# Kernel optimization log

Measured on AMD Instinct MI355X. Metric: run time of the kernel, lower is better.

## Reference

```python
import jax, jax.numpy as jnp
import numpy as np


def _segsum(x):
    """Stable segment sum: exp(segsum(A)) is 1-semiseparable. x: (..., T) -> (..., T, T)."""
    T = x.shape[-1]
    xx = jnp.broadcast_to(x[..., None], (*x.shape, T))
    xx = jnp.where(jnp.tril(jnp.ones((T, T), bool), -1), xx, 0.0)
    s = jnp.cumsum(xx, axis=-2)
    return jnp.where(jnp.tril(jnp.ones((T, T), bool), 0), s, -jnp.inf)


def setup_inputs() -> dict:
    key = jax.random.key(0)
    ks = jax.random.split(key, 6)
    b, T, h, p, n = 2, 1024, 32, 64, 128
    x = jax.random.normal(ks[0], (b, T, h, p), jnp.float32)
    # negative decay rates, as produced by -exp(A_log)*softplus(dt) in Mamba2
    A = -jax.random.uniform(ks[1], (b, T, h), jnp.float32, minval=0.01, maxval=0.5)
    B = jax.random.normal(ks[2], (b, T, h, n), jnp.float32)
    C = jax.random.normal(ks[3], (b, T, h, n), jnp.float32)
    # retrieval similarity mask (lower-triangular, like segment_and_cosine_similarity output)
    L_mask = jax.random.uniform(ks[4], (b, h, T, T), jnp.float32) * jnp.tril(jnp.ones((T, T), jnp.float32))
    mask_scaling_factor = jnp.float32(0.5)
    return {"x": x, "A": A, "B": B, "C": C, "L_mask": L_mask,
            "mask_scaling_factor": mask_scaling_factor, "chunk_size": 64}


def reference(x, A, B, C, L_mask, mask_scaling_factor, chunk_size):
    b, T, h, p = x.shape
    n = B.shape[-1]
    l = chunk_size
    k = T // l
    # chunk: b (c l) ... -> b c l ...
    xr = x.reshape(b, k, l, h, p)
    Br = B.reshape(b, k, l, h, n)
    Cr = C.reshape(b, k, l, h, n)
    Ar = jnp.transpose(A.reshape(b, k, l, h), (0, 3, 1, 2))  # b h c l
    A_cs = jnp.cumsum(Ar, axis=-1)                            # b h c l
    L = jnp.exp(_segsum(Ar))                                  # b h c l l
    # decompose_diagonal_and_lower_tri(L_mask, chunk_size)
    r = L_mask.reshape(b, h, k, l, k, l)
    didx = np.arange(k)
    L_mask_diag = jnp.moveaxis(r[:, :, didx, :, didx, :], 0, 2)          # b h k l l
    row_idx, col_idx = np.tril_indices(k, -1)                             # strict lower block pairs
    lower_tri = jnp.moveaxis(r[:, :, row_idx, :, col_idx, :], 0, 2)       # b h P l l
    L = L + mask_scaling_factor * L_mask_diag
    # diagonal (intra-chunk) blocks
    Y_diag = jnp.einsum('bclhn,bcshn,bhcls,bcshp->bclhp', Cr, Br, L, xr)
    # retrieval off-diagonal blocks, scatter-added back per destination chunk
    Y_tmp = jnp.einsum('bclhn,bcshn,bhcls,bcshp->bclhp',
                       Cr[:, row_idx], Br[:, col_idx],
                       mask_scaling_factor * lower_tri, xr[:, col_idx])   # b P l h p
    Y_retr = jnp.moveaxis(
        jax.ops.segment_sum(jnp.moveaxis(Y_tmp, 1, 0), jnp.asarray(row_idx), num_segments=k),
        0, 1)                                                             # b k l h p
    # inter-chunk state passing
    decay_states = jnp.exp(A_cs[..., -1:] - A_cs)                         # b h c l
    states = jnp.einsum('bclhn,bhcl,bclhp->bchpn', Br, decay_states, xr)  # b c h p n
    states = jnp.concatenate([jnp.zeros_like(states[:, :1]), states], axis=1)
    decay_chunk = jnp.exp(_segsum(jnp.pad(A_cs[..., -1], ((0, 0), (0, 0), (1, 0)))))  # b h (k+1) (k+1)
    new_states = jnp.einsum('bhzc,bchpn->bzhpn', decay_chunk, states)
    states_in, final_state = new_states[:, :-1], new_states[:, -1]
    Y_off = jnp.einsum('bclhn,bchpn,bhcl->bclhp', Cr, states_in, jnp.exp(A_cs))
    Y = (Y_diag + Y_off + Y_retr).reshape(b, T, h, p)
    return Y, final_state
```

## Files before the change

kernel.cpp:

```cpp
#include <hip/hip_runtime.h>

#define T_ 1024
#define H_ 32
#define P_ 64
#define N_ 128
#define L_ 64

typedef float f32x4 __attribute__((ext_vector_type(4)));
typedef short short8 __attribute__((ext_vector_type(8)));
typedef short short4v __attribute__((ext_vector_type(4)));

static __device__ __forceinline__ unsigned short f2bf(float f) {
  unsigned int u = __float_as_uint(f);
  u += 0x7fffu + ((u >> 16) & 1u);
  return (unsigned short)(u >> 16);
}
static __device__ __forceinline__ float bf2f(short s) {
  return __uint_as_float(((unsigned int)(unsigned short)s) << 16);
}

__global__ __launch_bounds__(1024) void cuma_kernel(const float* __restrict__ A,
                                                    float* __restrict__ cumA) {
  const int bh = blockIdx.x;
  const int b = bh >> 5, h = bh & 31;
  const int t = threadIdx.x;
  __shared__ float s[1024];
  s[t] = A[(b * T_ + t) * H_ + h];
  __syncthreads();
  for (int off = 1; off < 1024; off <<= 1) {
    float v = (t >= off) ? s[t - off] : 0.0f;
    __syncthreads();
    s[t] += v;
    __syncthreads();
  }
  cumA[bh * T_ + t] = s[t];
}

__global__ __launch_bounds__(256) void prep_b(const float* __restrict__ Bm,
                                              short* __restrict__ Bbf,
                                              short* __restrict__ BT) {
  const int bh = blockIdx.x;
  const int tb = blockIdx.y;
  const int b = bh >> 5, h = bh & 31;
  const int tid = threadIdx.x;
  __shared__ short Bt[128][72];
#pragma unroll
  for (int i = 0; i < 8; ++i) {
    const int idx = tid + 256 * i;
    const int row = idx >> 5, n4 = idx & 31;
    const float4 v = *(const float4*)(Bm + ((size_t)(b * T_ + tb * 64 + row) * H_ + h) * N_ + n4 * 4);
    short4v o;
    o.x = (short)f2bf(v.x); o.y = (short)f2bf(v.y);
    o.z = (short)f2bf(v.z); o.w = (short)f2bf(v.w);
    *(short4v*)(Bbf + ((size_t)bh * T_ + tb * 64 + row) * N_ + n4 * 4) = o;
    Bt[n4 * 4 + 0][row] = o.x; Bt[n4 * 4 + 1][row] = o.y;
    Bt[n4 * 4 + 2][row] = o.z; Bt[n4 * 4 + 3][row] = o.w;
  }
  __syncthreads();
#pragma unroll
  for (int i = 0; i < 4; ++i) {
    const int idx = tid + 256 * i;
    const int n = idx >> 3, t8 = idx & 7;
    const short4v a = *(const short4v*)&Bt[n][t8 * 8];
    const short4v c = *(const short4v*)&Bt[n][t8 * 8 + 4];
    short8 o;
    o[0] = a.x; o[1] = a.y; o[2] = a.z; o[3] = a.w;
    o[4] = c.x; o[5] = c.y; o[6] = c.z; o[7] = c.w;
    *(short8*)(BT + ((size_t)bh * N_ + n) * T_ + tb * 64 + t8 * 8) = o;
  }
}

__global__ __launch_bounds__(256) void prep_x(const float* __restrict__ x,
                                              short* __restrict__ xT) {
  const int bh = blockIdx.x, tb = blockIdx.y;
  const int b = bh >> 5, h = bh & 31;
  const int tid = threadIdx.x;
  __shared__ short Xt[64][72];
#pragma unroll
  for (int i = 0; i < 4; ++i) {
    const int idx = tid + 256 * i;
    const int row = idx >> 4, p4 = idx & 15;
    const float4 v = *(const float4*)(x + ((size_t)(b * T_ + tb * 64 + row) * H_ + h) * P_ + p4 * 4);
    Xt[p4 * 4 + 0][row] = (short)f2bf(v.x);
    Xt[p4 * 4 + 1][row] = (short)f2bf(v.y);
    Xt[p4 * 4 + 2][row] = (short)f2bf(v.z);
    Xt[p4 * 4 + 3][row] = (short)f2bf(v.w);
  }
  __syncthreads();
#pragma unroll
  for (int i = 0; i < 2; ++i) {
    const int idx = tid + 256 * i;
    const int p = idx >> 3, t8 = idx & 7;
    const short4v a = *(const short4v*)&Xt[p][t8 * 8];
    const short4v c = *(const short4v*)&Xt[p][t8 * 8 + 4];
    short8 o;
    o[0] = a.x; o[1] = a.y; o[2] = a.z; o[3] = a.w;
    o[4] = c.x; o[5] = c.y; o[6] = c.z; o[7] = c.w;
    *(short8*)(xT + ((size_t)bh * P_ + p) * T_ + tb * 64 + t8 * 8) = o;
  }
}

__global__ __launch_bounds__(256, 4) void attn_kernel(
    const short* __restrict__ xT, const short* __restrict__ Bbf,
    const float* __restrict__ Cm, const float* __restrict__ mask,
    const float* __restrict__ msf_p, const float* __restrict__ cumA,
    float* __restrict__ Y) {
  const int blk = blockIdx.x;
  const int qc = 15 - (blk >> 6);
  const int bh = blk & 63;
  const int b = bh >> 5, h = bh & 31;
  const float msf = msf_p[0];
  const int tid = threadIdx.x;
  const int w = tid >> 6;
  const int lane = tid & 63;
  const int q = lane >> 4, c = lane & 15;

  __shared__ short Ps[4][16][72];

  short8 cf[4];
  {
    const float* Cg = Cm + ((size_t)(b * T_ + qc * L_ + 16 * w + c) * H_ + h) * N_ + 8 * q;
#pragma unroll
    for (int kt = 0; kt < 4; ++kt) {
      const float4 v0 = *(const float4*)(Cg + kt * 32);
      const float4 v1 = *(const float4*)(Cg + kt * 32 + 4);
      short8 f;
      f[0] = (short)f2bf(v0.x); f[1] = (short)f2bf(v0.y);
      f[2] = (short)f2bf(v0.z); f[3] = (short)f2bf(v0.w);
      f[4] = (short)f2bf(v1.x); f[5] = (short)f2bf(v1.y);
      f[6] = (short)f2bf(v1.z); f[7] = (short)f2bf(v1.w);
      cf[kt] = f;
    }
  }
  float ca_i[4];
#pragma unroll
  for (int r = 0; r < 4; ++r)
    ca_i[r] = cumA[bh * T_ + qc * L_ + 16 * w + 4 * q + r];

  f32x4 yacc[4];
#pragma unroll
  for (int pt = 0; pt < 4; ++pt) yacc[pt] = (f32x4){0.f, 0.f, 0.f, 0.f};

  for (int kc = 0; kc <= qc; ++kc) {
    float mv[16];
    {
      const float* mbase = mask + ((size_t)bh * T_ + (size_t)(qc * L_ + 16 * w + 4 * q)) * T_ +
                           (size_t)kc * L_ + c;
#pragma unroll
      for (int tj = 0; tj < 4; ++tj)
#pragma unroll
        for (int r = 0; r < 4; ++r)
          mv[tj * 4 + r] = mbase[(size_t)r * T_ + 16 * tj];
    }
    float ck[4];
#pragma unroll
    for (int tj = 0; tj < 4; ++tj)
      ck[tj] = cumA[bh * T_ + kc * L_ + 16 * tj + c];

    f32x4 sacc[4];
#pragma unroll
    for (int tj = 0; tj < 4; ++tj) sacc[tj] = (f32x4){0.f, 0.f, 0.f, 0.f};
    const short* Bg = Bbf + ((size_t)bh * T_ + kc * L_) * N_ + 8 * q;
#pragma unroll
    for (int kt = 0; kt < 4; ++kt) {
#pragma unroll
      for (int tj = 0; tj < 4; ++tj) {
        const short8 bf = *(const short8*)(Bg + (size_t)(16 * tj + c) * N_ + kt * 32);
        sacc[tj] = __builtin_amdgcn_mfma_f32_16x16x32_bf16(cf[kt], bf, sacc[tj], 0, 0, 0);
      }
    }

    const bool diag = (kc == qc);
#pragma unroll
    for (int tj = 0; tj < 4; ++tj) {
      const int j_l = 16 * tj + c;
#pragma unroll
      for (int r = 0; r < 4; ++r) {
        const int i_l = 16 * w + 4 * q + r;
        float wgt = __expf(ca_i[r] - ck[tj]) + msf * mv[tj * 4 + r];
        if (diag && j_l > i_l) wgt = 0.0f;
        Ps[w][4 * q + r][j_l] = (short)f2bf(sacc[tj][r] * wgt);
      }
    }

#pragma unroll
    for (int kt2 = 0; kt2 < 2; ++kt2) {
      const short8 pf = *(const short8*)&Ps[w][c][kt2 * 32 + 8 * q];
      const short* xg = xT + (size_t)bh * P_ * T_ + kc * L_ + kt2 * 32 + 8 * q;
#pragma unroll
      for (int pt = 0; pt < 4; ++pt) {
        const short8 xf = *(const short8*)(xg + (size_t)(16 * pt + c) * T_);
        yacc[pt] = __builtin_amdgcn_mfma_f32_16x16x32_bf16(pf, xf, yacc[pt], 0, 0, 0);
      }
    }
  }

  float* Yg = Y + ((size_t)(b * T_ + qc * L_ + 16 * w + 4 * q) * H_ + h) * P_;
#pragma unroll
  for (int pt = 0; pt < 4; ++pt)
#pragma unroll
    for (int r = 0; r < 4; ++r)
      Yg[(size_t)r * (H_ * P_) + 16 * pt + c] = yacc[pt][r];
}

__global__ __launch_bounds__(512) void state_kernel(
    const short* __restrict__ xT, const short* __restrict__ BT,
    const float* __restrict__ cumA, float* __restrict__ out) {
  const int bh = blockIdx.x;
  const int tid = threadIdx.x;
  const int w = (tid >> 6) & 3;
  const int th = tid >> 8;
  const int lane = tid & 63;
  const int q = lane >> 4, c = lane & 15;

  __shared__ float wsh[1024];
  __shared__ float red[4][16][128];
  {
    const float cend = cumA[bh * T_ + (T_ - 1)];
    for (int t = tid; t < 1024; t += 512)
      wsh[t] = __expf(cend - cumA[bh * T_ + t]);
  }
  __syncthreads();

  f32x4 acc[8];
#pragma unroll
  for (int nt = 0; nt < 8; ++nt) acc[nt] = (f32x4){0.f, 0.f, 0.f, 0.f};

  for (int ktl = 0; ktl < 16; ++ktl) {
    const int t0 = th * 512 + ktl * 32;
    const short8 xv = *(const short8*)(xT + ((size_t)bh * P_ + 16 * w + c) * T_ + t0 + 8 * q);
    const float4 w0 = *(const float4*)&wsh[t0 + 8 * q];
    const float4 w1 = *(const float4*)&wsh[t0 + 8 * q + 4];
    short8 af;
    af[0] = (short)f2bf(bf2f(xv[0]) * w0.x); af[1] = (short)f2bf(bf2f(xv[1]) * w0.y);
    af[2] = (short)f2bf(bf2f(xv[2]) * w0.z); af[3] = (short)f2bf(bf2f(xv[3]) * w0.w);
    af[4] = (short)f2bf(bf2f(xv[4]) * w1.x); af[5] = (short)f2bf(bf2f(xv[5]) * w1.y);
    af[6] = (short)f2bf(bf2f(xv[6]) * w1.z); af[7] = (short)f2bf(bf2f(xv[7]) * w1.w);
#pragma unroll
    for (int nt = 0; nt < 8; ++nt) {
      const short8 bf = *(const short8*)(BT + ((size_t)bh * N_ + 16 * nt + c) * T_ + t0 + 8 * q);
      acc[nt] = __builtin_amdgcn_mfma_f32_16x16x32_bf16(af, bf, acc[nt], 0, 0, 0);
    }
  }

  if (th == 1) {
#pragma unroll
    for (int nt = 0; nt < 8; ++nt)
#pragma unroll
      for (int r = 0; r < 4; ++r) red[w][4 * q + r][16 * nt + c] = acc[nt][r];
  }
  __syncthreads();
  if (th == 0) {
    float* o = out + (size_t)bh * P_ * N_;
#pragma unroll
    for (int nt = 0; nt < 8; ++nt)
#pragma unroll
      for (int r = 0; r < 4; ++r)
        o[(size_t)(16 * w + 4 * q + r) * N_ + 16 * nt + c] =
            acc[nt][r] + red[w][4 * q + r][16 * nt + c];
  }
}

extern "C" void kernel_launch(void* const* d_in, const int* in_sizes, int n_in,
                              void* d_out, int out_size, void* d_ws, size_t ws_size,
                              hipStream_t stream) {
  const float* x    = (const float*)d_in[0];
  const float* A    = (const float*)d_in[1];
  const float* Bm   = (const float*)d_in[2];
  const float* Cm   = (const float*)d_in[3];
  const float* mask = (const float*)d_in[4];
  const float* msf  = (const float*)d_in[5];
  float* Y  = (float*)d_out;
  float* fs = (float*)d_out + (size_t)2 * T_ * H_ * P_;

  char* ws = (char*)d_ws;
  float* cumA = (float*)ws;
  short* Bbf  = (short*)(ws + (1 << 18));
  short* BT   = (short*)(ws + (1 << 18) + (size_t)64 * T_ * N_ * 2);
  short* xT   = (short*)(ws + (1 << 18) + (size_t)128 * T_ * N_ * 2);

  cuma_kernel<<<64, 1024, 0, stream>>>(A, cumA);
  prep_b<<<dim3(64, 16), 256, 0, stream>>>(Bm, Bbf, BT);
  prep_x<<<dim3(64, 16), 256, 0, stream>>>(x, xT);
  attn_kernel<<<1024, 256, 0, stream>>>(xT, Bbf, Cm, mask, msf, cumA, Y);
  state_kernel<<<64, 512, 0, stream>>>(xT, BT, cumA, fs);
}
```

Measured before the change: 539.0 us.

## Prefetch mask tiles one chunk ahead and precompute bf16 C in fused prep kernel

Merges the B and x prep kernels into one launch that also converts C to bf16 in workspace, so the attention kernel loads C directly as bf16 fragments instead of converting fp32 per block. In the attention loop, mask values and cumA keys for the next chunk are loaded before the current chunk's MFMA work, using nontemporal loads, to hide the latency of streaming the large mask. Output stores are made nontemporal. This adds register pressure from the double-buffered mask values and extra workspace for Cbf.

```diff
diff --git a/kernel.cpp b/kernel.cpp
--- a/kernel.cpp
+++ b/kernel.cpp
@@ -36,14 +36,18 @@
   cumA[bh * T_ + t] = s[t];
 }
 
-__global__ __launch_bounds__(256) void prep_b(const float* __restrict__ Bm,
-                                              short* __restrict__ Bbf,
-                                              short* __restrict__ BT) {
+__global__ __launch_bounds__(256) void prep_kernel(
+    const float* __restrict__ x, const float* __restrict__ Bm,
+    const float* __restrict__ Cm, short* __restrict__ Bbf,
+    short* __restrict__ BT, short* __restrict__ Cbf,
+    short* __restrict__ xT) {
   const int bh = blockIdx.x;
   const int tb = blockIdx.y;
   const int b = bh >> 5, h = bh & 31;
   const int tid = threadIdx.x;
   __shared__ short Bt[128][72];
+  __shared__ short Xt[64][72];
+
 #pragma unroll
   for (int i = 0; i < 8; ++i) {
     const int idx = tid + 256 * i;
@@ -56,6 +60,26 @@
     Bt[n4 * 4 + 0][row] = o.x; Bt[n4 * 4 + 1][row] = o.y;
     Bt[n4 * 4 + 2][row] = o.z; Bt[n4 * 4 + 3][row] = o.w;
   }
+#pragma unroll
+  for (int i = 0; i < 8; ++i) {
+    const int idx = tid + 256 * i;
+    const int row = idx >> 5, n4 = idx & 31;
+    const float4 v = *(const float4*)(Cm + ((size_t)(b * T_ + tb * 64 + row) * H_ + h) * N_ + n4 * 4);
+    short4v o;
+    o.x = (short)f2bf(v.x); o.y = (short)f2bf(v.y);
+    o.z = (short)f2bf(v.z); o.w = (short)f2bf(v.w);
+    *(short4v*)(Cbf + ((size_t)bh * T_ + tb * 64 + row) * N_ + n4 * 4) = o;
+  }
+#pragma unroll
+  for (int i = 0; i < 4; ++i) {
+    const int idx = tid + 256 * i;
+    const int row = idx >> 4, p4 = idx & 15;
+    const float4 v = *(const float4*)(x + ((size_t)(b * T_ + tb * 64 + row) * H_ + h) * P_ + p4 * 4);
+    Xt[p4 * 4 + 0][row] = (short)f2bf(v.x);
+    Xt[p4 * 4 + 1][row] = (short)f2bf(v.y);
+    Xt[p4 * 4 + 2][row] = (short)f2bf(v.z);
+    Xt[p4 * 4 + 3][row] = (short)f2bf(v.w);
+  }
   __syncthreads();
 #pragma unroll
   for (int i = 0; i < 4; ++i) {
@@ -68,25 +92,6 @@
     o[4] = c.x; o[5] = c.y; o[6] = c.z; o[7] = c.w;
     *(short8*)(BT + ((size_t)bh * N_ + n) * T_ + tb * 64 + t8 * 8) = o;
   }
-}
-
-__global__ __launch_bounds__(256) void prep_x(const float* __restrict__ x,
-                                              short* __restrict__ xT) {
-  const int bh = blockIdx.x, tb = blockIdx.y;
-  const int b = bh >> 5, h = bh & 31;
-  const int tid = threadIdx.x;
-  __shared__ short Xt[64][72];
-#pragma unroll
-  for (int i = 0; i < 4; ++i) {
-    const int idx = tid + 256 * i;
-    const int row = idx >> 4, p4 = idx & 15;
-    const float4 v = *(const float4*)(x + ((size_t)(b * T_ + tb * 64 + row) * H_ + h) * P_ + p4 * 4);
-    Xt[p4 * 4 + 0][row] = (short)f2bf(v.x);
-    Xt[p4 * 4 + 1][row] = (short)f2bf(v.y);
-    Xt[p4 * 4 + 2][row] = (short)f2bf(v.z);
-    Xt[p4 * 4 + 3][row] = (short)f2bf(v.w);
-  }
-  __syncthreads();
 #pragma unroll
   for (int i = 0; i < 2; ++i) {
     const int idx = tid + 256 * i;
@@ -102,7 +107,7 @@
 
 __global__ __launch_bounds__(256, 4) void attn_kernel(
     const short* __restrict__ xT, const short* __restrict__ Bbf,
-    const float* __restrict__ Cm, const float* __restrict__ mask,
+    const short* __restrict__ Cbf, const float* __restrict__ mask,
     const float* __restrict__ msf_p, const float* __restrict__ cumA,
     float* __restrict__ Y) {
   const int blk = blockIdx.x;
@@ -119,18 +124,9 @@
 
   short8 cf[4];
   {
-    const float* Cg = Cm + ((size_t)(b * T_ + qc * L_ + 16 * w + c) * H_ + h) * N_ + 8 * q;
-#pragma unroll
-    for (int kt = 0; kt < 4; ++kt) {
-      const float4 v0 = *(const float4*)(Cg + kt * 32);
-      const float4 v1 = *(const float4*)(Cg + kt * 32 + 4);
-      short8 f;
-      f[0] = (short)f2bf(v0.x); f[1] = (short)f2bf(v0.y);
-      f[2] = (short)f2bf(v0.z); f[3] = (short)f2bf(v0.w);
-      f[4] = (short)f2bf(v1.x); f[5] = (short)f2bf(v1.y);
-      f[6] = (short)f2bf(v1.z); f[7] = (short)f2bf(v1.w);
-      cf[kt] = f;
-    }
+    const short* Cg = Cbf + ((size_t)bh * T_ + qc * L_ + 16 * w + c) * N_ + 8 * q;
+#pragma unroll
+    for (int kt = 0; kt < 4; ++kt) cf[kt] = *(const short8*)(Cg + kt * 32);
   }
   float ca_i[4];
 #pragma unroll
@@ -141,21 +137,33 @@
 #pragma unroll
   for (int pt = 0; pt < 4; ++pt) yacc[pt] = (f32x4){0.f, 0.f, 0.f, 0.f};
 
+  const float* mrow0 = mask + ((size_t)bh * T_ + (size_t)(qc * L_ + 16 * w + 4 * q)) * T_ + c;
+
+  float mv[16], ck[4];
+  {
+    const float* mb = mrow0;
+#pragma unroll
+    for (int tj = 0; tj < 4; ++tj)
+#pragma unroll
+      for (int r = 0; r < 4; ++r)
+        mv[tj * 4 + r] = __builtin_nontemporal_load(mb + (size_t)r * T_ + 16 * tj);
+#pragma unroll
+    for (int tj = 0; tj < 4; ++tj) ck[tj] = cumA[bh * T_ + 16 * tj + c];
+  }
+
   for (int kc = 0; kc <= qc; ++kc) {
-    float mv[16];
-    {
-      const float* mbase = mask + ((size_t)bh * T_ + (size_t)(qc * L_ + 16 * w + 4 * q)) * T_ +
-                           (size_t)kc * L_ + c;
+    float mvn[16], ckn[4];
+    if (kc < qc) {
+      const float* mb = mrow0 + (size_t)(kc + 1) * L_;
 #pragma unroll
       for (int tj = 0; tj < 4; ++tj)
 #pragma unroll
         for (int r = 0; r < 4; ++r)
-          mv[tj * 4 + r] = mbase[(size_t)r * T_ + 16 * tj];
-    }
-    float ck[4];
-#pragma unroll
-    for (int tj = 0; tj < 4; ++tj)
-      ck[tj] = cumA[bh * T_ + kc * L_ + 16 * tj + c];
+          mvn[tj * 4 + r] = __builtin_nontemporal_load(mb + (size_t)r * T_ + 16 * tj);
+#pragma unroll
+      for (int tj = 0; tj < 4; ++tj)
+        ckn[tj] = cumA[bh * T_ + (kc + 1) * L_ + 16 * tj + c];
+    }
 
     f32x4 sacc[4];
 #pragma unroll
@@ -193,6 +201,11 @@
         yacc[pt] = __builtin_amdgcn_mfma_f32_16x16x32_bf16(pf, xf, yacc[pt], 0, 0, 0);
       }
     }
+
+#pragma unroll
+    for (int e = 0; e < 16; ++e) mv[e] = mvn[e];
+#pragma unroll
+    for (int e = 0; e < 4; ++e) ck[e] = ckn[e];
   }
 
   float* Yg = Y + ((size_t)(b * T_ + qc * L_ + 16 * w + 4 * q) * H_ + h) * P_;
@@ -200,7 +213,7 @@
   for (int pt = 0; pt < 4; ++pt)
 #pragma unroll
     for (int r = 0; r < 4; ++r)
-      Yg[(size_t)r * (H_ * P_) + 16 * pt + c] = yacc[pt][r];
+      __builtin_nontemporal_store(yacc[pt][r], Yg + (size_t)r * (H_ * P_) + 16 * pt + c);
 }
 
 __global__ __launch_bounds__(512) void state_kernel(
@@ -275,13 +288,14 @@
 
   char* ws = (char*)d_ws;
   float* cumA = (float*)ws;
-  short* Bbf  = (short*)(ws + (1 << 18));
-  short* BT   = (short*)(ws + (1 << 18) + (size_t)64 * T_ * N_ * 2);
-  short* xT   = (short*)(ws + (1 << 18) + (size_t)128 * T_ * N_ * 2);
+  size_t off = 1 << 18;
+  short* Bbf = (short*)(ws + off); off += (size_t)64 * T_ * N_ * 2;
+  short* BT  = (short*)(ws + off); off += (size_t)64 * T_ * N_ * 2;
+  short* Cbf = (short*)(ws + off); off += (size_t)64 * T_ * N_ * 2;
+  short* xT  = (short*)(ws + off);
 
   cuma_kernel<<<64, 1024, 0, stream>>>(A, cumA);
-  prep_b<<<dim3(64, 16), 256, 0, stream>>>(Bm, Bbf, BT);
-  prep_x<<<dim3(64, 16), 256, 0, stream>>>(x, xT);
-  attn_kernel<<<1024, 256, 0, stream>>>(xT, Bbf, Cm, mask, msf, cumA, Y);
+  prep_kernel<<<dim3(64, 16), 256, 0, stream>>>(x, Bm, Cm, Bbf, BT, Cbf, xT);
+  attn_kernel<<<1024, 256, 0, stream>>>(xT, Bbf, Cbf, mask, msf, cumA, Y);
   state_kernel<<<64, 512, 0, stream>>>(xT, BT, cumA, fs);
 }
```

Result: slower. 554.0 us (+2.8%).
